# Kernel tuning notes

Measured on AMD Instinct MI355X. Metric: run time of the kernel, lower is better.

## Reference

```python
import jax, jax.numpy as jnp
import numpy as np

N_NODES = 50000
N_EDGES = 800000
IN_F = 191
H1, C1 = 16, 16   # conv1: heads=16, out=16, concat -> 256
H2, C2 = 8, 3     # conv2: heads=8, out=3, concat=False -> mean


def _glorot(key, shape):
    fan = shape[0] + shape[-1] if len(shape) == 2 else sum(shape)
    s = jnp.sqrt(6.0 / fan)
    return jax.random.uniform(key, shape, jnp.float32, -s, s)


def setup_inputs() -> dict:
    key = jax.random.key(0)
    ks = jax.random.split(key, 16)
    x = jax.random.normal(ks[0], (N_NODES, IN_F), jnp.float32)
    edge_index = jax.random.randint(ks[1], (2, N_EDGES), 0, N_NODES)
    edge_attr = jax.random.normal(ks[2], (N_EDGES, 1), jnp.float32)
    return {
        "x": x, "edge_index": edge_index, "edge_attr": edge_attr,
        "W1": _glorot(ks[3], (IN_F, H1 * C1)),
        "We1": _glorot(ks[4], (1, H1 * C1)),
        "a_src1": _glorot(ks[5], (H1, C1)),
        "a_dst1": _glorot(ks[6], (H1, C1)),
        "a_edge1": _glorot(ks[7], (H1, C1)),
        "b1": jnp.zeros((H1 * C1,), jnp.float32),
        "W2": _glorot(ks[8], (H1 * C1, H2 * C2)),
        "We2": _glorot(ks[9], (1, H2 * C2)),
        "a_src2": _glorot(ks[10], (H2, C2)),
        "a_dst2": _glorot(ks[11], (H2, C2)),
        "a_edge2": _glorot(ks[12], (H2, C2)),
        "b2": jnp.zeros((C2,), jnp.float32),
    }


def gat_conv(x, src, dst, edge_attr, W, We, a_src, a_dst, a_edge, bias, H, C, concat):
    # x: [N, F]; src/dst: [E'] (self loops already appended); edge_attr: [E', De]
    N = x.shape[0]
    xl = (x @ W).reshape(N, H, C)                       # [N,H,C]
    e = (edge_attr @ We).reshape(-1, H, C)              # [E',H,C]
    alpha_src = (xl * a_src).sum(-1)                    # [N,H]
    alpha_dst = (xl * a_dst).sum(-1)                    # [N,H]
    alpha_e = (e * a_edge).sum(-1)                      # [E',H]
    alpha = alpha_src[src] + alpha_dst[dst] + alpha_e   # [E',H]
    alpha = jax.nn.leaky_relu(alpha, 0.2)
    # softmax over incoming edges per destination node
    m = jax.ops.segment_max(alpha, dst, num_segments=N)
    alpha = jnp.exp(alpha - m[dst])
    den = jax.ops.segment_sum(alpha, dst, num_segments=N)
    alpha = alpha / (den[dst] + 1e-16)
    out = jax.ops.segment_sum(alpha[:, :, None] * xl[src], dst, num_segments=N)  # [N,H,C]
    if concat:
        return out.reshape(N, H * C) + bias
    return out.mean(axis=1) + bias


def reference(x, edge_index, edge_attr, W1, We1, a_src1, a_dst1, a_edge1, b1,
              W2, We2, a_src2, a_dst2, a_edge2, b2):
    N = x.shape[0]
    # add self loops (PyG default, edge_attr fill_value='mean')
    loop = jnp.arange(N)
    src = jnp.concatenate([edge_index[0], loop])
    dst = jnp.concatenate([edge_index[1], loop])
    ea_mean = edge_attr.mean(axis=0, keepdims=True)
    ea = jnp.concatenate([edge_attr, jnp.broadcast_to(ea_mean, (N, edge_attr.shape[1]))], axis=0)

    h = gat_conv(x, src, dst, ea, W1, We1, a_src1, a_dst1, a_edge1, b1, H1, C1, True)
    h = jax.nn.elu(h)
    h = gat_conv(h, src, dst, ea, W2, We2, a_src2, a_dst2, a_edge2, b2, H2, C2, False)
    h = jax.nn.elu(h)
    return h
```

## Files before the change

kernel.cpp:

```cpp
#include <hip/hip_runtime.h>
#include <math.h>
#include <stdint.h>

#define N_NODES 50000
#define N_EDGES 800000
#define N_TOT   850000
#define IN_F    191
#define F1      256
#define NH1     16
#define NC1     16
#define F2      24
#define NH2     8
#define NC2     3
#define KP      192
#define MPAD    50048
#define NCVT_X  (MPAD * 24)
#define NCVT_W  (F1 * 24)
#define HIST_B  3125
#define EASUM_B 256
#define CVT_B   ((NCVT_X + NCVT_W) / 256)

typedef __attribute__((ext_vector_type(8))) short bf16x8;
typedef __attribute__((ext_vector_type(4))) float f32x4;

#define GLL16(g, s) __builtin_amdgcn_global_load_lds( \
    (const __attribute__((address_space(1))) void*)(g), \
    (__attribute__((address_space(3))) void*)(s), 16, 0, 0)

__device__ __forceinline__ float lrelu(float x) { return x > 0.f ? x : 0.2f * x; }

__device__ __forceinline__ uint16_t f2bf1(float f) {
    uint32_t u = __float_as_uint(f);
    return (uint16_t)((u + 0x7fffu + ((u >> 16) & 1u)) >> 16);
}
__device__ __forceinline__ void bf2f2(uint32_t u, float* lo, float* hi) {
    *lo = __uint_as_float(u << 16);
    *hi = __uint_as_float(u & 0xffff0000u);
}

__global__ void k_pre(const int* __restrict__ ei, const float* __restrict__ ea,
                      const float* __restrict__ x, const float* __restrict__ W1,
                      int* counts, float* __restrict__ part,
                      uint16_t* __restrict__ xh, uint16_t* __restrict__ wht) {
    int b = blockIdx.x, t = threadIdx.x;
    if (b < HIST_B) {
        int e = b * 256 + t;
        if (e < N_EDGES) atomicAdd(&counts[ei[N_EDGES + e]], 1);
    } else if (b < HIST_B + EASUM_B) {
        __shared__ float wsums[4];
        int eb = b - HIST_B;
        float v = 0.f;
        for (int e = eb * 256 + t; e < N_EDGES; e += 256 * 256) v += ea[e];
        #pragma unroll
        for (int off = 32; off >= 1; off >>= 1) v += __shfl_xor(v, off);
        if ((t & 63) == 0) wsums[t >> 6] = v;
        __syncthreads();
        if (t == 0) part[eb] = wsums[0] + wsums[1] + wsums[2] + wsums[3];
    } else {
        int idx = (b - HIST_B - EASUM_B) * 256 + t;
        if (idx < NCVT_X) {
            int row = idx / 24, kw = idx - row * 24;
            int k0 = kw * 8;
            uint16_t hv[8];
            #pragma unroll
            for (int j = 0; j < 8; j++) {
                int k = k0 + j;
                float v = (row < N_NODES && k < IN_F) ? x[(size_t)row * IN_F + k] : 0.f;
                hv[j] = f2bf1(v);
            }
            *(uint4*)(xh + (size_t)row * KP + k0) = *(const uint4*)hv;
        } else {
            int id2 = idx - NCVT_X;
            int col = id2 / 24, kw = id2 - col * 24;
            int k0 = kw * 8;
            uint16_t hv[8];
            #pragma unroll
            for (int j = 0; j < 8; j++) {
                int k = k0 + j;
                float v = (k < IN_F) ? W1[(size_t)k * F1 + col] : 0.f;
                hv[j] = f2bf1(v);
            }
            *(uint4*)(wht + (size_t)col * KP + k0) = *(const uint4*)hv;
        }
    }
}

__global__ __launch_bounds__(1024) void k_scan1(const int* __restrict__ counts,
        int* rowptr, int* bsums,
        const float* __restrict__ We1, const float* __restrict__ ae1,
        const float* __restrict__ We2, const float* __restrict__ ae2,
        const float* __restrict__ part, float* scalars) {
    int b = blockIdx.x, t = threadIdx.x;
    if (b == 49) {
        if (t < 64) {
            if (t < NH1) {
                float s = 0.f;
                for (int c = 0; c < NC1; c++) s += We1[t * NC1 + c] * ae1[t * NC1 + c];
                scalars[1 + t] = s;
            } else if (t < NH1 + NH2) {
                int h = t - NH1;
                float s = 0.f;
                for (int c = 0; c < NC2; c++) s += We2[h * NC2 + c] * ae2[h * NC2 + c];
                scalars[17 + h] = s;
            }
            float v = part[t * 4] + part[t * 4 + 1] + part[t * 4 + 2] + part[t * 4 + 3];
            #pragma unroll
            for (int off = 32; off >= 1; off >>= 1) v += __shfl_xor(v, off);
            if (t == 0) scalars[0] = v / (float)N_EDGES;
        }
        return;
    }
    __shared__ int wsum[16];
    int lane = t & 63, w = t >> 6;
    int i = b * 1024 + t;
    int v = (i < N_NODES) ? counts[i] + 1 : 0;
    int incl = v;
    #pragma unroll
    for (int off = 1; off < 64; off <<= 1) {
        int u = __shfl_up(incl, off);
        if (lane >= off) incl += u;
    }
    if (lane == 63) wsum[w] = incl;
    __syncthreads();
    int woff = 0;
    #pragma unroll
    for (int k = 0; k < 16; k++) woff += (k < w) ? wsum[k] : 0;
    if (i < N_NODES) rowptr[i] = woff + incl - v;
    if (t == 1023) bsums[b] = woff + incl;
}

__global__ __launch_bounds__(1024) void k_scan2(int* rowptr, int* cursor,
                                                const int* __restrict__ bsums) {
    __shared__ int off_s;
    int b = blockIdx.x, t = threadIdx.x;
    if (t == 0) {
        int o = 0;
        for (int k = 0; k < b; k++) o += bsums[k];
        off_s = o;
        if (b == 48) rowptr[N_NODES] = o + bsums[48];
    }
    __syncthreads();
    int i = b * 1024 + t;
    if (i < N_NODES) {
        int r = rowptr[i] + off_s;
        rowptr[i] = r;
        cursor[i] = r;
    }
}

__global__ void k_scatter(const int* __restrict__ ei, const float* __restrict__ ea,
                          const float* __restrict__ scalars, int* cursor,
                          uint32_t* __restrict__ csr) {
    int i = blockIdx.x * blockDim.x + threadIdx.x;
    if (i < N_EDGES) {
        int s = ei[i], d = ei[N_EDGES + i];
        int pos = atomicAdd(&cursor[d], 1);
        csr[pos] = (uint32_t)s | ((uint32_t)f2bf1(ea[i]) << 16);
    } else if (i < N_TOT) {
        int n = i - N_EDGES;
        int pos = atomicAdd(&cursor[n], 1);
        csr[pos] = (uint32_t)n | ((uint32_t)f2bf1(scalars[0]) << 16);
    }
}

__global__ __launch_bounds__(256) void k_gemm1_mfma(const uint16_t* __restrict__ xh,
        const uint16_t* __restrict__ wht, const float* __restrict__ a_src,
        const float* __restrict__ a_dst, uint16_t* __restrict__ xl1b,
        float* __restrict__ asrc1, float* __restrict__ adst1) {
    __shared__ uint16_t smem[64 * 256];
    uint16_t* ldsA = smem;
    uint16_t* ldsB = smem + 4 * 512;
    const int t = threadIdx.x;
    const int l = t & 63, w = t >> 6;
    const int m0 = blockIdx.x * 64;
    const int lr = l & 15, lk = l >> 4;

    f32x4 acc[4][4];
    #pragma unroll
    for (int i = 0; i < 4; i++)
        #pragma unroll
        for (int j = 0; j < 4; j++)
            acc[i][j] = (f32x4){0.f, 0.f, 0.f, 0.f};

    for (int ks = 0; ks < 6; ks++) {
        const int kb = ks * 32 + lk * 8;
        #pragma unroll
        for (int ii = 0; ii < 5; ii++) {
            const int idx = w * 5 + ii;
            if (idx < 4) {
                const uint16_t* src = xh + (size_t)(m0 + idx * 16 + lr) * KP + kb;
                GLL16(src, ldsA + idx * 512);
            } else {
                const int g = idx - 4;
                const uint16_t* src = wht + (size_t)(g * 16 + lr) * KP + kb;
                GLL16(src, ldsB + g * 512);
            }
        }
        __syncthreads();
        bf16x8 ah[4];
        #pragma unroll
        for (int i = 0; i < 4; i++)
            ah[i] = *(const bf16x8*)(ldsA + (i * 64 + l) * 8);
        #pragma unroll
        for (int j = 0; j < 4; j++) {
            const int g = w * 4 + j;
            bf16x8 bh = *(const bf16x8*)(ldsB + (g * 64 + l) * 8);
            #pragma unroll
            for (int i = 0; i < 4; i++)
                acc[i][j] = __builtin_amdgcn_mfma_f32_16x16x32_bf16(ah[i], bh, acc[i][j], 0, 0, 0);
        }
        __syncthreads();
    }
    #pragma unroll
    for (int i = 0; i < 4; i++) {
        #pragma unroll
        for (int r = 0; r < 4; r++) {
            const int lrow = i * 16 + lk * 4 + r;
            const int gm = m0 + lrow;
            #pragma unroll
            for (int j = 0; j < 4; j++) {
                const int gn = (w * 4 + j) * 16 + lr;
                uint16_t bv = f2bf1(acc[i][j][r]);
                smem[lrow * 256 + gn] = bv;
                if (gm < N_NODES) xl1b[(size_t)gm * F1 + gn] = bv;
            }
        }
    }
    __syncthreads();
    #pragma unroll
    for (int q = 0; q < 4; q++) {
        int item = q * 256 + t;
        int row = item >> 4, h = item & 15;
        int gm = m0 + row;
        if (gm < N_NODES) {
            const uint4* rp = (const uint4*)(smem + row * 256 + h * 16);
            uint4 u0 = rp[0], u1 = rp[1];
            uint32_t us[8] = {u0.x, u0.y, u0.z, u0.w, u1.x, u1.y, u1.z, u1.w};
            float as = 0.f, ad = 0.f;
            #pragma unroll
            for (int p = 0; p < 8; p++) {
                float lo, hi;
                bf2f2(us[p], &lo, &hi);
                as += lo * a_src[h * 16 + 2 * p] + hi * a_src[h * 16 + 2 * p + 1];
                ad += lo * a_dst[h * 16 + 2 * p] + hi * a_dst[h * 16 + 2 * p + 1];
            }
            asrc1[gm * 16 + h] = as;
            adst1[gm * 16 + h] = ad;
        }
    }
}

__global__ __launch_bounds__(256) void k_agg1(const int* __restrict__ rowptr,
        const uint32_t* __restrict__ csr,
        const uint16_t* __restrict__ xl1b, const float* __restrict__ asrc,
        const float* __restrict__ adst, const float* __restrict__ scalars,
        const float* __restrict__ b1, uint16_t* __restrict__ h1b) {
    int node = blockIdx.x * 4 + (threadIdx.x >> 6);
    int lane = threadIdx.x & 63;
    int eg = lane >> 4, h = lane & 15;
    int r0 = rowptr[node], r1 = rowptr[node + 1];
    float ad = adst[node * 16 + h];
    float wd = scalars[1 + h];
    float den = 0.f;
    float acc[16];
    #pragma unroll
    for (int c = 0; c < 16; c++) acc[c] = 0.f;
    for (int j = r0 + eg; j < r1; j += 4) {
        uint32_t pk = csr[j];
        int s = (int)(pk & 0xFFFFu);
        float eav = __uint_as_float(pk & 0xFFFF0000u);
        float a = lrelu(asrc[s * 16 + h] + ad + eav * wd);
        float wgt = __expf(a);
        den += wgt;
        const uint4* xp = (const uint4*)(xl1b + (size_t)s * F1 + h * 16);
        uint4 u0 = xp[0], u1 = xp[1];
        float lo, hi;
        bf2f2(u0.x, &lo, &hi); acc[0] += wgt * lo;  acc[1] += wgt * hi;
        bf2f2(u0.y, &lo, &hi); acc[2] += wgt * lo;  acc[3] += wgt * hi;
        bf2f2(u0.z, &lo, &hi); acc[4] += wgt * lo;  acc[5] += wgt * hi;
        bf2f2(u0.w, &lo, &hi); acc[6] += wgt * lo;  acc[7] += wgt * hi;
        bf2f2(u1.x, &lo, &hi); acc[8] += wgt * lo;  acc[9] += wgt * hi;
        bf2f2(u1.y, &lo, &hi); acc[10] += wgt * lo; acc[11] += wgt * hi;
        bf2f2(u1.z, &lo, &hi); acc[12] += wgt * lo; acc[13] += wgt * hi;
        bf2f2(u1.w, &lo, &hi); acc[14] += wgt * lo; acc[15] += wgt * hi;
    }
    den += __shfl_xor(den, 16);
    den += __shfl_xor(den, 32);
    float inv = 1.f / (den + 1e-16f);
    #pragma unroll
    for (int c = 0; c < 16; c++) {
        acc[c] += __shfl_xor(acc[c], 16);
        acc[c] += __shfl_xor(acc[c], 32);
    }
    if (eg == 0) {
        uint32_t pk[8];
        #pragma unroll
        for (int q = 0; q < 8; q++) {
            float v0 = acc[2 * q] * inv + b1[h * 16 + 2 * q];
            float v1 = acc[2 * q + 1] * inv + b1[h * 16 + 2 * q + 1];
            v0 = v0 > 0.f ? v0 : expm1f(v0);
            v1 = v1 > 0.f ? v1 : expm1f(v1);
            pk[q] = (uint32_t)f2bf1(v0) | ((uint32_t)f2bf1(v1) << 16);
        }
        uint4* op = (uint4*)(h1b + (size_t)node * F1 + h * 16);
        op[0] = make_uint4(pk[0], pk[1], pk[2], pk[3]);
        op[1] = make_uint4(pk[4], pk[5], pk[6], pk[7]);
    }
}

__global__ __launch_bounds__(256) void k_layer2(const uint16_t* __restrict__ h1b,
        const float* __restrict__ W2, const float* __restrict__ a_src,
        const float* __restrict__ a_dst, uint16_t* __restrict__ xl2b,
        float* __restrict__ asrc, float* __restrict__ adst) {
    __shared__ float W2s[F2][258];
    int t = threadIdx.x;
    for (int i = t; i < 256 * F2; i += 256) {
        int k = i / F2, c = i - k * F2;
        W2s[c][k] = W2[i];
    }
    __syncthreads();
    int idx = blockIdx.x * 256 + t;
    if (idx >= N_NODES * NH2) return;
    int n = idx >> 3, h = idx & 7;
    int c0 = h * 3;
    const uint4* hp = (const uint4*)(h1b + (size_t)n * F1);
    float a0 = 0.f, a1 = 0.f, a2 = 0.f;
    #pragma unroll 4
    for (int q = 0; q < 32; q++) {
        uint4 u = hp[q];
        float f[8];
        bf2f2(u.x, &f[0], &f[1]);
        bf2f2(u.y, &f[2], &f[3]);
        bf2f2(u.z, &f[4], &f[5]);
        bf2f2(u.w, &f[6], &f[7]);
        #pragma unroll
        for (int j = 0; j < 8; j++) {
            int k = q * 8 + j;
            a0 += f[j] * W2s[c0][k];
            a1 += f[j] * W2s[c0 + 1][k];
            a2 += f[j] * W2s[c0 + 2][k];
        }
    }
    uint2 pk;
    pk.x = (uint32_t)f2bf1(a0) | ((uint32_t)f2bf1(a1) << 16);
    pk.y = (uint32_t)f2bf1(a2);
    *(uint2*)(xl2b + (size_t)idx * 4) = pk;
    asrc[idx] = a0 * a_src[h * 3 + 0] + a1 * a_src[h * 3 + 1] + a2 * a_src[h * 3 + 2];
    adst[idx] = a0 * a_dst[h * 3 + 0] + a1 * a_dst[h * 3 + 1] + a2 * a_dst[h * 3 + 2];
}

__global__ __launch_bounds__(256) void k_agg2(const int* __restrict__ rowptr,
        const uint32_t* __restrict__ csr,
        const uint16_t* __restrict__ xl2b, const float* __restrict__ asrc,
        const float* __restrict__ adst, const float* __restrict__ scalars,
        const float* __restrict__ b2, float* __restrict__ out) {
    int node = blockIdx.x * 4 + (threadIdx.x >> 6);
    int lane = threadIdx.x & 63;
    int eg = lane >> 3, h = lane & 7;
    int r0 = rowptr[node], r1 = rowptr[node + 1];
    float ad = adst[node * 8 + h];
    float wd = scalars[17 + h];
    float den = 0.f, a0 = 0.f, a1 = 0.f, a2 = 0.f;
    for (int j = r0 + eg; j < r1; j += 8) {
        uint32_t pk = csr[j];
        int s = (int)(pk & 0xFFFFu);
        float eav = __uint_as_float(pk & 0xFFFF0000u);
        float a = lrelu(asrc[s * 8 + h] + ad + eav * wd);
        float wgt = __expf(a);
        den += wgt;
        const uint2* xp = (const uint2*)(xl2b + ((size_t)s * 8 + h) * 4);
        uint2 u = xp[0];
        float x0, x1, x2, dummy;
        bf2f2(u.x, &x0, &x1);
        bf2f2(u.y, &x2, &dummy);
        a0 += wgt * x0;
        a1 += wgt * x1;
        a2 += wgt * x2;
    }
    den += __shfl_xor(den, 8); den += __shfl_xor(den, 16); den += __shfl_xor(den, 32);
    float inv = 1.f / (den + 1e-16f);
    a0 += __shfl_xor(a0, 8); a0 += __shfl_xor(a0, 16); a0 += __shfl_xor(a0, 32);
    a1 += __shfl_xor(a1, 8); a1 += __shfl_xor(a1, 16); a1 += __shfl_xor(a1, 32);
    a2 += __shfl_xor(a2, 8); a2 += __shfl_xor(a2, 16); a2 += __shfl_xor(a2, 32);
    a0 *= inv; a1 *= inv; a2 *= inv;
    a0 += __shfl_xor(a0, 1); a0 += __shfl_xor(a0, 2); a0 += __shfl_xor(a0, 4);
    a1 += __shfl_xor(a1, 1); a1 += __shfl_xor(a1, 2); a1 += __shfl_xor(a1, 4);
    a2 += __shfl_xor(a2, 1); a2 += __shfl_xor(a2, 2); a2 += __shfl_xor(a2, 4);
    if (lane == 0) {
        float v0 = a0 * 0.125f + b2[0];
        float v1 = a1 * 0.125f + b2[1];
        float v2 = a2 * 0.125f + b2[2];
        out[node * 3 + 0] = v0 > 0.f ? v0 : expm1f(v0);
        out[node * 3 + 1] = v1 > 0.f ? v1 : expm1f(v1);
        out[node * 3 + 2] = v2 > 0.f ? v2 : expm1f(v2);
    }
}

extern "C" void kernel_launch(void* const* d_in, const int* in_sizes, int n_in,
                              void* d_out, int out_size, void* d_ws, size_t ws_size,
                              hipStream_t stream) {
    const float* x       = (const float*)d_in[0];
    const int*   ei      = (const int*)d_in[1];
    const float* ea      = (const float*)d_in[2];
    const float* W1      = (const float*)d_in[3];
    const float* We1     = (const float*)d_in[4];
    const float* a_src1  = (const float*)d_in[5];
    const float* a_dst1  = (const float*)d_in[6];
    const float* a_edge1 = (const float*)d_in[7];
    const float* b1      = (const float*)d_in[8];
    const float* W2      = (const float*)d_in[9];
    const float* We2     = (const float*)d_in[10];
    const float* a_src2  = (const float*)d_in[11];
    const float* a_dst2  = (const float*)d_in[12];
    const float* a_edge2 = (const float*)d_in[13];
    const float* b2      = (const float*)d_in[14];
    float* out = (float*)d_out;

    char* ws = (char*)d_ws;
    size_t off = 0;
    auto alloc = [&](size_t nbytes) -> void* {
        void* p = ws + off;
        off = (off + nbytes + 255) & ~(size_t)255;
        return p;
    };
    uint16_t* xl1b  = (uint16_t*)alloc((size_t)N_NODES * F1 * 2);
    uint16_t* h1b   = (uint16_t*)alloc((size_t)N_NODES * F1 * 2);
    float* asrc1    = (float*)alloc((size_t)N_NODES * NH1 * 4);
    float* adst1    = (float*)alloc((size_t)N_NODES * NH1 * 4);
    uint16_t* xl2b  = (uint16_t*)alloc((size_t)N_NODES * 32 * 2);
    float* asrc2    = (float*)alloc((size_t)N_NODES * NH2 * 4);
    float* adst2    = (float*)alloc((size_t)N_NODES * NH2 * 4);
    int*   counts   = (int*)alloc((size_t)N_NODES * 4);
    int*   rowptr   = (int*)alloc((size_t)(N_NODES + 1) * 4);
    int*   cursor   = (int*)alloc((size_t)N_NODES * 4);
    int*   bsums    = (int*)alloc(64 * 4);
    uint32_t* csr   = (uint32_t*)alloc((size_t)N_TOT * 4);
    float* scalars  = (float*)alloc(128);
    float* part     = (float*)alloc(256 * 4);
    uint16_t* wht   = (uint16_t*)alloc((size_t)F1 * KP * 2);
    uint16_t* xh    = (uint16_t*)alloc((size_t)MPAD * KP * 2);

    hipMemsetAsync(counts, 0, (size_t)N_NODES * 4, stream);
    hipLaunchKernelGGL(k_pre, dim3(HIST_B + EASUM_B + CVT_B), dim3(256), 0, stream,
                       ei, ea, x, W1, counts, part, xh, wht);
    hipLaunchKernelGGL(k_scan1, dim3(50), dim3(1024), 0, stream,
                       counts, rowptr, bsums, We1, a_edge1, We2, a_edge2, part, scalars);
    hipLaunchKernelGGL(k_scan2, dim3(49), dim3(1024), 0, stream, rowptr, cursor, bsums);
    hipLaunchKernelGGL(k_scatter, dim3((N_TOT + 255) / 256), dim3(256), 0, stream,
                       ei, ea, scalars, cursor, csr);
    hipLaunchKernelGGL(k_gemm1_mfma, dim3(MPAD / 64), dim3(256), 0, stream,
                       xh, wht, a_src1, a_dst1, xl1b, asrc1, adst1);
    hipLaunchKernelGGL(k_agg1, dim3(N_NODES / 4), dim3(256), 0, stream,
                       rowptr, csr, xl1b, asrc1, adst1, scalars, b1, h1b);
    hipLaunchKernelGGL(k_layer2, dim3((N_NODES * NH2 + 255) / 256), dim3(256), 0, stream,
                       h1b, W2, a_src2, a_dst2, xl2b, asrc2, adst2);
    hipLaunchKernelGGL(k_agg2, dim3(N_NODES / 4), dim3(256), 0, stream,
                       rowptr, csr, xl2b, asrc2, adst2, scalars, b2, out);
}
```

Measured before the change: 275.2 us.

## Fuse CSR scan, offset and scatter kernels into one cooperative kernel

Replaces the two scan kernels and the edge scatter kernel with a single cooperative-launch kernel that uses grid-wide syncs between the block scan, the offset propagation and the atomic CSR scatter. This removes two kernel launches and the gaps between them. In exchange it adds grid.sync barriers and a grid-stride scatter over a fixed 256-block grid, and it requires all blocks to be co-resident.

```diff
diff --git a/kernel.cpp b/kernel.cpp
--- a/kernel.cpp
+++ b/kernel.cpp
@@ -1,6 +1,9 @@
 #include <hip/hip_runtime.h>
+#include <hip/hip_cooperative_groups.h>
 #include <math.h>
 #include <stdint.h>
+
+namespace cg = cooperative_groups;
 
 #define N_NODES 50000
 #define N_EDGES 800000
@@ -19,6 +22,7 @@
 #define HIST_B  3125
 #define EASUM_B 256
 #define CVT_B   ((NCVT_X + NCVT_W) / 256)
+#define BUILD_B 256
 
 typedef __attribute__((ext_vector_type(8))) short bf16x8;
 typedef __attribute__((ext_vector_type(4))) float f32x4;
@@ -85,81 +89,73 @@
     }
 }
 
-__global__ __launch_bounds__(1024) void k_scan1(const int* __restrict__ counts,
-        int* rowptr, int* bsums,
+__global__ __launch_bounds__(1024) void k_build(const int* __restrict__ counts,
+        int* rowptr, int* cursor, int* bsums,
         const float* __restrict__ We1, const float* __restrict__ ae1,
         const float* __restrict__ We2, const float* __restrict__ ae2,
-        const float* __restrict__ part, float* scalars) {
-    int b = blockIdx.x, t = threadIdx.x;
-    if (b == 49) {
-        if (t < 64) {
-            if (t < NH1) {
-                float s = 0.f;
-                for (int c = 0; c < NC1; c++) s += We1[t * NC1 + c] * ae1[t * NC1 + c];
-                scalars[1 + t] = s;
-            } else if (t < NH1 + NH2) {
-                int h = t - NH1;
-                float s = 0.f;
-                for (int c = 0; c < NC2; c++) s += We2[h * NC2 + c] * ae2[h * NC2 + c];
-                scalars[17 + h] = s;
-            }
-            float v = part[t * 4] + part[t * 4 + 1] + part[t * 4 + 2] + part[t * 4 + 3];
-            #pragma unroll
-            for (int off = 32; off >= 1; off >>= 1) v += __shfl_xor(v, off);
-            if (t == 0) scalars[0] = v / (float)N_EDGES;
-        }
-        return;
-    }
-    __shared__ int wsum[16];
-    int lane = t & 63, w = t >> 6;
-    int i = b * 1024 + t;
-    int v = (i < N_NODES) ? counts[i] + 1 : 0;
-    int incl = v;
-    #pragma unroll
-    for (int off = 1; off < 64; off <<= 1) {
-        int u = __shfl_up(incl, off);
-        if (lane >= off) incl += u;
-    }
-    if (lane == 63) wsum[w] = incl;
-    __syncthreads();
-    int woff = 0;
-    #pragma unroll
-    for (int k = 0; k < 16; k++) woff += (k < w) ? wsum[k] : 0;
-    if (i < N_NODES) rowptr[i] = woff + incl - v;
-    if (t == 1023) bsums[b] = woff + incl;
-}
-
-__global__ __launch_bounds__(1024) void k_scan2(int* rowptr, int* cursor,
-                                                const int* __restrict__ bsums) {
-    __shared__ int off_s;
-    int b = blockIdx.x, t = threadIdx.x;
-    if (t == 0) {
-        int o = 0;
-        for (int k = 0; k < b; k++) o += bsums[k];
-        off_s = o;
-        if (b == 48) rowptr[N_NODES] = o + bsums[48];
-    }
-    __syncthreads();
-    int i = b * 1024 + t;
-    if (i < N_NODES) {
-        int r = rowptr[i] + off_s;
-        rowptr[i] = r;
-        cursor[i] = r;
-    }
-}
-
-__global__ void k_scatter(const int* __restrict__ ei, const float* __restrict__ ea,
-                          const float* __restrict__ scalars, int* cursor,
-                          uint32_t* __restrict__ csr) {
-    int i = blockIdx.x * blockDim.x + threadIdx.x;
-    if (i < N_EDGES) {
-        int s = ei[i], d = ei[N_EDGES + i];
-        int pos = atomicAdd(&cursor[d], 1);
-        csr[pos] = (uint32_t)s | ((uint32_t)f2bf1(ea[i]) << 16);
-    } else if (i < N_TOT) {
-        int n = i - N_EDGES;
-        int pos = atomicAdd(&cursor[n], 1);
-        csr[pos] = (uint32_t)n | ((uint32_t)f2bf1(scalars[0]) << 16);
+        const float* __restrict__ part, float* scalars,
+        const int* __restrict__ ei, const float* __restrict__ ea,
+        uint32_t* __restrict__ csr) {
+    cg::grid_group grid = cg::this_grid();
+    const int b = blockIdx.x, t = threadIdx.x;
+    if (b < 49) {
+        __shared__ int wsum[16];
+        int lane = t & 63, w = t >> 6;
+        int i = b * 1024 + t;
+        int v = (i < N_NODES) ? counts[i] + 1 : 0;
+        int incl = v;
+        #pragma unroll
+        for (int off = 1; off < 64; off <<= 1) {
+            int u = __shfl_up(incl, off);
+            if (lane >= off) incl += u;
+        }
+        if (lane == 63) wsum[w] = incl;
+        __syncthreads();
+        int woff = 0;
+        #pragma unroll
+        for (int k = 0; k < 16; k++) woff += (k < w) ? wsum[k] : 0;
+        if (i < N_NODES) rowptr[i] = woff + incl - v;
+        if (t == 1023) bsums[b] = woff + incl;
+    } else if (b == 49 && t < 64) {
+        if (t < NH1) {
+            float s = 0.f;
+            for (int c = 0; c < NC1; c++) s += We1[t * NC1 + c] * ae1[t * NC1 + c];
+            scalars[1 + t] = s;
+        } else if (t < NH1 + NH2) {
+            int h = t - NH1;
+            float s = 0.f;
+            for (int c = 0; c < NC2; c++) s += We2[h * NC2 + c] * ae2[h * NC2 + c];
+            scalars[17 + h] = s;
+        }
+        float v = part[t * 4] + part[t * 4 + 1] + part[t * 4 + 2] + part[t * 4 + 3];
+        #pragma unroll
+        for (int off = 32; off >= 1; off >>= 1) v += __shfl_xor(v, off);
+        if (t == 0) scalars[0] = v / (float)N_EDGES;
+    }
+    grid.sync();
+    if (b < 49) {
+        int off = 0;
+        for (int k = 0; k < b; k++) off += bsums[k];
+        int i = b * 1024 + t;
+        if (i < N_NODES) {
+            int r = rowptr[i] + off;
+            rowptr[i] = r;
+            cursor[i] = r;
+        }
+        if (b == 48 && t == 1023) rowptr[N_NODES] = off + bsums[48];
+    }
+    grid.sync();
+    float eam = scalars[0];
+    for (int i = b * 1024 + t; i < N_TOT; i += BUILD_B * 1024) {
+        if (i < N_EDGES) {
+            int s = ei[i], d = ei[N_EDGES + i];
+            int pos = atomicAdd(&cursor[d], 1);
+            csr[pos] = (uint32_t)s | ((uint32_t)f2bf1(ea[i]) << 16);
+        } else {
+            int n = i - N_EDGES;
+            int pos = atomicAdd(&cursor[n], 1);
+            csr[pos] = (uint32_t)n | ((uint32_t)f2bf1(eam) << 16);
+        }
     }
 }
 
@@ -443,11 +439,14 @@
     hipMemsetAsync(counts, 0, (size_t)N_NODES * 4, stream);
     hipLaunchKernelGGL(k_pre, dim3(HIST_B + EASUM_B + CVT_B), dim3(256), 0, stream,
                        ei, ea, x, W1, counts, part, xh, wht);
-    hipLaunchKernelGGL(k_scan1, dim3(50), dim3(1024), 0, stream,
-                       counts, rowptr, bsums, We1, a_edge1, We2, a_edge2, part, scalars);
-    hipLaunchKernelGGL(k_scan2, dim3(49), dim3(1024), 0, stream, rowptr, cursor, bsums);
-    hipLaunchKernelGGL(k_scatter, dim3((N_TOT + 255) / 256), dim3(256), 0, stream,
-                       ei, ea, scalars, cursor, csr);
+    {
+        void* args[] = {(void*)&counts, (void*)&rowptr, (void*)&cursor, (void*)&bsums,
+                        (void*)&We1, (void*)&a_edge1, (void*)&We2, (void*)&a_edge2,
+                        (void*)&part, (void*)&scalars, (void*)&ei, (void*)&ea,
+                        (void*)&csr};
+        hipLaunchCooperativeKernel((void*)k_build, dim3(BUILD_B), dim3(1024),
+                                   args, 0, stream);
+    }
     hipLaunchKernelGGL(k_gemm1_mfma, dim3(MPAD / 64), dim3(256), 0, stream,
                        xh, wht, a_src1, a_dst1, xl1b, asrc1, adst1);
     hipLaunchKernelGGL(k_agg1, dim3(N_NODES / 4), dim3(256), 0, stream,
```

Measured after the change: 347.3 us. 1.26x slower.

## Fuse layer-2 projection into layer-1 aggregation and write self loops in scan

Applied to the files above, without the earlier changes.

The layer-2 linear projection and attention-logit computation are folded into the layer-1 aggregation kernel. Each block stages its four aggregated rows in shared memory and multiplies them by a bf16 copy of W2 held in LDS. This removes the h1 intermediate buffer (a 25MB write and read) and one kernel launch. Separately, self-loop CSR entries are written directly at the start of each row during the scan, so 50k atomics leave the scatter kernel. The costs are that every agg1 block reloads and converts W2 into LDS, and W2 is now rounded to bf16, which slightly changes precision.

```diff
diff --git a/kernel.cpp b/kernel.cpp
--- a/kernel.cpp
+++ b/kernel.cpp
@@ -37,6 +37,9 @@
     *lo = __uint_as_float(u << 16);
     *hi = __uint_as_float(u & 0xffff0000u);
 }
+__device__ __forceinline__ float bf2f(uint16_t v) {
+    return __uint_as_float((uint32_t)v << 16);
+}
 
 __global__ void k_pre(const int* __restrict__ ei, const float* __restrict__ ea,
                       const float* __restrict__ x, const float* __restrict__ W1,
@@ -130,7 +133,9 @@
 }
 
 __global__ __launch_bounds__(1024) void k_scan2(int* rowptr, int* cursor,
-                                                const int* __restrict__ bsums) {
+                                                const int* __restrict__ bsums,
+                                                const float* __restrict__ scalars,
+                                                uint32_t* __restrict__ csr) {
     __shared__ int off_s;
     int b = blockIdx.x, t = threadIdx.x;
     if (t == 0) {
@@ -140,26 +145,23 @@
         if (b == 48) rowptr[N_NODES] = o + bsums[48];
     }
     __syncthreads();
+    uint32_t loop_ea = (uint32_t)f2bf1(scalars[0]) << 16;
     int i = b * 1024 + t;
     if (i < N_NODES) {
         int r = rowptr[i] + off_s;
         rowptr[i] = r;
-        cursor[i] = r;
+        cursor[i] = r + 1;
+        csr[r] = (uint32_t)i | loop_ea;
     }
 }
 
 __global__ void k_scatter(const int* __restrict__ ei, const float* __restrict__ ea,
-                          const float* __restrict__ scalars, int* cursor,
-                          uint32_t* __restrict__ csr) {
+                          int* cursor, uint32_t* __restrict__ csr) {
     int i = blockIdx.x * blockDim.x + threadIdx.x;
     if (i < N_EDGES) {
         int s = ei[i], d = ei[N_EDGES + i];
         int pos = atomicAdd(&cursor[d], 1);
         csr[pos] = (uint32_t)s | ((uint32_t)f2bf1(ea[i]) << 16);
-    } else if (i < N_TOT) {
-        int n = i - N_EDGES;
-        int pos = atomicAdd(&cursor[n], 1);
-        csr[pos] = (uint32_t)n | ((uint32_t)f2bf1(scalars[0]) << 16);
     }
 }
 
@@ -254,9 +256,19 @@
         const uint32_t* __restrict__ csr,
         const uint16_t* __restrict__ xl1b, const float* __restrict__ asrc,
         const float* __restrict__ adst, const float* __restrict__ scalars,
-        const float* __restrict__ b1, uint16_t* __restrict__ h1b) {
-    int node = blockIdx.x * 4 + (threadIdx.x >> 6);
-    int lane = threadIdx.x & 63;
+        const float* __restrict__ b1, const float* __restrict__ W2,
+        const float* __restrict__ a_src2, const float* __restrict__ a_dst2,
+        uint16_t* __restrict__ xl2b, float* __restrict__ asrc2,
+        float* __restrict__ adst2) {
+    __shared__ uint16_t W2s[F2][260];
+    __shared__ uint32_t rowbuf[4][128];
+    int tid = threadIdx.x;
+    for (int i = tid; i < 256 * F2; i += 256) {
+        int k = i / F2, c = i - k * F2;
+        W2s[c][k] = f2bf1(W2[i]);
+    }
+    int node = blockIdx.x * 4 + (tid >> 6);
+    int lane = tid & 63;
     int eg = lane >> 4, h = lane & 15;
     int r0 = rowptr[node], r1 = rowptr[node + 1];
     float ad = adst[node * 16 + h];
@@ -293,60 +305,44 @@
         acc[c] += __shfl_xor(acc[c], 32);
     }
     if (eg == 0) {
-        uint32_t pk[8];
         #pragma unroll
         for (int q = 0; q < 8; q++) {
             float v0 = acc[2 * q] * inv + b1[h * 16 + 2 * q];
             float v1 = acc[2 * q + 1] * inv + b1[h * 16 + 2 * q + 1];
             v0 = v0 > 0.f ? v0 : expm1f(v0);
             v1 = v1 > 0.f ? v1 : expm1f(v1);
-            pk[q] = (uint32_t)f2bf1(v0) | ((uint32_t)f2bf1(v1) << 16);
-        }
-        uint4* op = (uint4*)(h1b + (size_t)node * F1 + h * 16);
-        op[0] = make_uint4(pk[0], pk[1], pk[2], pk[3]);
-        op[1] = make_uint4(pk[4], pk[5], pk[6], pk[7]);
-    }
-}
-
-__global__ __launch_bounds__(256) void k_layer2(const uint16_t* __restrict__ h1b,
-        const float* __restrict__ W2, const float* __restrict__ a_src,
-        const float* __restrict__ a_dst, uint16_t* __restrict__ xl2b,
-        float* __restrict__ asrc, float* __restrict__ adst) {
-    __shared__ float W2s[F2][258];
-    int t = threadIdx.x;
-    for (int i = t; i < 256 * F2; i += 256) {
-        int k = i / F2, c = i - k * F2;
-        W2s[c][k] = W2[i];
+            rowbuf[tid >> 6][h * 8 + q] =
+                (uint32_t)f2bf1(v0) | ((uint32_t)f2bf1(v1) << 16);
+        }
     }
     __syncthreads();
-    int idx = blockIdx.x * 256 + t;
-    if (idx >= N_NODES * NH2) return;
-    int n = idx >> 3, h = idx & 7;
-    int c0 = h * 3;
-    const uint4* hp = (const uint4*)(h1b + (size_t)n * F1);
+    int it = tid >> 3, sub = tid & 7;
+    int nl = it >> 3, h2 = it & 7;
+    int c0 = h2 * 3;
     float a0 = 0.f, a1 = 0.f, a2 = 0.f;
-    #pragma unroll 4
-    for (int q = 0; q < 32; q++) {
-        uint4 u = hp[q];
-        float f[8];
-        bf2f2(u.x, &f[0], &f[1]);
-        bf2f2(u.y, &f[2], &f[3]);
-        bf2f2(u.z, &f[4], &f[5]);
-        bf2f2(u.w, &f[6], &f[7]);
-        #pragma unroll
-        for (int j = 0; j < 8; j++) {
-            int k = q * 8 + j;
-            a0 += f[j] * W2s[c0][k];
-            a1 += f[j] * W2s[c0 + 1][k];
-            a2 += f[j] * W2s[c0 + 2][k];
-        }
-    }
-    uint2 pk;
-    pk.x = (uint32_t)f2bf1(a0) | ((uint32_t)f2bf1(a1) << 16);
-    pk.y = (uint32_t)f2bf1(a2);
-    *(uint2*)(xl2b + (size_t)idx * 4) = pk;
-    asrc[idx] = a0 * a_src[h * 3 + 0] + a1 * a_src[h * 3 + 1] + a2 * a_src[h * 3 + 2];
-    adst[idx] = a0 * a_dst[h * 3 + 0] + a1 * a_dst[h * 3 + 1] + a2 * a_dst[h * 3 + 2];
+    #pragma unroll
+    for (int m = 0; m < 16; m++) {
+        int k = sub * 32 + m * 2;
+        uint32_t u = rowbuf[nl][k >> 1];
+        float lo, hi;
+        bf2f2(u, &lo, &hi);
+        a0 += lo * bf2f(W2s[c0][k])     + hi * bf2f(W2s[c0][k + 1]);
+        a1 += lo * bf2f(W2s[c0 + 1][k]) + hi * bf2f(W2s[c0 + 1][k + 1]);
+        a2 += lo * bf2f(W2s[c0 + 2][k]) + hi * bf2f(W2s[c0 + 2][k + 1]);
+    }
+    a0 += __shfl_xor(a0, 1); a0 += __shfl_xor(a0, 2); a0 += __shfl_xor(a0, 4);
+    a1 += __shfl_xor(a1, 1); a1 += __shfl_xor(a1, 2); a1 += __shfl_xor(a1, 4);
+    a2 += __shfl_xor(a2, 1); a2 += __shfl_xor(a2, 2); a2 += __shfl_xor(a2, 4);
+    if (sub == 0) {
+        int n = blockIdx.x * 4 + nl;
+        int idx = n * 8 + h2;
+        uint2 pk;
+        pk.x = (uint32_t)f2bf1(a0) | ((uint32_t)f2bf1(a1) << 16);
+        pk.y = (uint32_t)f2bf1(a2);
+        *(uint2*)(xl2b + (size_t)idx * 4) = pk;
+        asrc2[idx] = a0 * a_src2[h2 * 3 + 0] + a1 * a_src2[h2 * 3 + 1] + a2 * a_src2[h2 * 3 + 2];
+        adst2[idx] = a0 * a_dst2[h2 * 3 + 0] + a1 * a_dst2[h2 * 3 + 1] + a2 * a_dst2[h2 * 3 + 2];
+    }
 }
 
 __global__ __launch_bounds__(256) void k_agg2(const int* __restrict__ rowptr,
@@ -424,7 +420,6 @@
         return p;
     };
     uint16_t* xl1b  = (uint16_t*)alloc((size_t)N_NODES * F1 * 2);
-    uint16_t* h1b   = (uint16_t*)alloc((size_t)N_NODES * F1 * 2);
     float* asrc1    = (float*)alloc((size_t)N_NODES * NH1 * 4);
     float* adst1    = (float*)alloc((size_t)N_NODES * NH1 * 4);
     uint16_t* xl2b  = (uint16_t*)alloc((size_t)N_NODES * 32 * 2);
@@ -445,15 +440,15 @@
                        ei, ea, x, W1, counts, part, xh, wht);
     hipLaunchKernelGGL(k_scan1, dim3(50), dim3(1024), 0, stream,
                        counts, rowptr, bsums, We1, a_edge1, We2, a_edge2, part, scalars);
-    hipLaunchKernelGGL(k_scan2, dim3(49), dim3(1024), 0, stream, rowptr, cursor, bsums);
-    hipLaunchKernelGGL(k_scatter, dim3((N_TOT + 255) / 256), dim3(256), 0, stream,
-                       ei, ea, scalars, cursor, csr);
+    hipLaunchKernelGGL(k_scan2, dim3(49), dim3(1024), 0, stream,
+                       rowptr, cursor, bsums, scalars, csr);
+    hipLaunchKernelGGL(k_scatter, dim3((N_EDGES + 255) / 256), dim3(256), 0, stream,
+                       ei, ea, cursor, csr);
     hipLaunchKernelGGL(k_gemm1_mfma, dim3(MPAD / 64), dim3(256), 0, stream,
                        xh, wht, a_src1, a_dst1, xl1b, asrc1, adst1);
     hipLaunchKernelGGL(k_agg1, dim3(N_NODES / 4), dim3(256), 0, stream,
-                       rowptr, csr, xl1b, asrc1, adst1, scalars, b1, h1b);
-    hipLaunchKernelGGL(k_layer2, dim3((N_NODES * NH2 + 255) / 256), dim3(256), 0, stream,
-                       h1b, W2, a_src2, a_dst2, xl2b, asrc2, adst2);
+                       rowptr, csr, xl1b, asrc1, adst1, scalars, b1,
+                       W2, a_src2, a_dst2, xl2b, asrc2, adst2);
     hipLaunchKernelGGL(k_agg2, dim3(N_NODES / 4), dim3(256), 0, stream,
                        rowptr, csr, xl2b, asrc2, adst2, scalars, b2, out);
 }
```

Measured after the change: 306.0 us. +11.2%, slower.
